# Kernel tuning notes

Hardware: AMD Instinct MI355X
Metric: run time of the kernel (lower is better)

Reference implementation:

```python
import jax, jax.numpy as jnp
import numpy as np
import math

B, T, D, H = 2, 2048, 1024, 16


def _layernorm(x, gamma, beta, eps=1e-5):
    mu = jnp.mean(x, axis=-1, keepdims=True)
    var = jnp.var(x, axis=-1, keepdims=True)
    return (x - mu) * jax.lax.rsqrt(var + eps) * gamma + beta


def setup_inputs() -> dict:
    key = jax.random.key(0)
    ks = jax.random.split(key, 12)
    s = 1.0 / math.sqrt(D)
    return {
        "x": jax.random.normal(ks[0], (B, T, D), dtype=jnp.float32),
        "src_mask": jax.random.randint(ks[1], (B, T, T), 0, 2, dtype=jnp.int32),
        "ln_gamma": jnp.ones((D,), jnp.float32),
        "ln_beta": jnp.zeros((D,), jnp.float32),
        "Wq": jax.random.normal(ks[2], (D, D), jnp.float32) * s,
        "bq": jnp.zeros((D,), jnp.float32),
        "Wk": jax.random.normal(ks[3], (D, D), jnp.float32) * s,
        "bk": jnp.zeros((D,), jnp.float32),
        "Wv": jax.random.normal(ks[4], (D, D), jnp.float32) * s,
        "bv": jnp.zeros((D,), jnp.float32),
        "Wo": jax.random.normal(ks[5], (D, D), jnp.float32) * s,
        "bo": jnp.zeros((D,), jnp.float32),
    }


def reference(x, src_mask, ln_gamma, ln_beta, Wq, bq, Wk, bk, Wv, bv, Wo, bo):
    Bx, Tx, Dx = x.shape
    dh = Dx // H
    xn = _layernorm(x, ln_gamma, ln_beta)  # single LN; the three calls are identical
    q = (xn @ Wq + bq).reshape(Bx, Tx, H, dh)
    k = (xn @ Wk + bk).reshape(Bx, Tx, H, dh)
    v = (xn @ Wv + bv).reshape(Bx, Tx, H, dh)
    # scores: B, n, m, h
    attn = jnp.einsum('bnhd,bmhd->bnmh', q, k) / math.sqrt(dh)
    attn = attn + (1.0 - src_mask.astype(attn.dtype))[..., None] * -100000.0
    weight = jax.nn.softmax(attn, axis=2)
    y = jnp.einsum('bnmh,bmhd->bnhd', weight, v).reshape(Bx, Tx, Dx)
    return x + (y @ Wo + bo)
```

## Files before the change

kernel.cpp:

```cpp
#include <hip/hip_runtime.h>
#include <hip/hip_bf16.h>
#include <stdint.h>

#define Tq 2048
#define Dd 1024
#define Hh 16

typedef unsigned short u16;
typedef __attribute__((ext_vector_type(8))) short short8;
typedef __attribute__((ext_vector_type(4))) float f32x4;

__device__ __forceinline__ u16 f2bf(float f) {
  union { float f; unsigned u; } v; v.f = f;
  unsigned r = (v.u + 0x7fffu + ((v.u >> 16) & 1u)) >> 16;
  return (u16)r;
}

__device__ __forceinline__ unsigned pk2bf(float a, float b) {
  __hip_bfloat162 h = __float22bfloat162_rn(float2{a, b});
  union { __hip_bfloat162 h; unsigned u; } c; c.h = h;
  return c.u;
}

__device__ __forceinline__ void load_lds16(const void* g, void* l) {
  __builtin_amdgcn_global_load_lds(
      (const __attribute__((address_space(1))) unsigned*)g,
      (__attribute__((address_space(3))) unsigned*)l, 16, 0, 0);
}

__device__ __forceinline__ f32x4 mfma16(short8 a, short8 b, f32x4 c) {
  return __builtin_amdgcn_mfma_f32_16x16x32_bf16(a, b, c, 0, 0, 0);
}

__device__ __forceinline__ void permswap(unsigned& xx, unsigned& yy) {
#if __has_builtin(__builtin_amdgcn_permlane32_swap) && \
    __has_builtin(__builtin_amdgcn_permlane16_swap)
  typedef __attribute__((ext_vector_type(2))) unsigned uint2v;
  uint2v t0 = __builtin_amdgcn_permlane32_swap(xx, yy, false, false);
  uint2v t1 = __builtin_amdgcn_permlane16_swap(t0[0], t0[1], false, false);
  xx = t1[0];
  yy = t1[1];
#else
  asm volatile(
      "s_nop 1\n\t"
      "v_permlane32_swap_b32 %0, %1\n\t"
      "s_nop 1\n\t"
      "v_permlane16_swap_b32 %0, %1\n\t"
      "s_nop 1"
      : "+v"(xx), "+v"(yy));
#endif
}

__global__ __launch_bounds__(256) void prep_kernel(
    const float* __restrict__ x, const float* __restrict__ gamma,
    const float* __restrict__ beta, u16* __restrict__ xn,
    const float* __restrict__ W0, const float* __restrict__ W1,
    const float* __restrict__ W2, const float* __restrict__ W3,
    u16* __restrict__ o_qkv, u16* __restrict__ o_o,
    const int* __restrict__ mask, uint32_t* __restrict__ bits,
    const float* __restrict__ bq, const float* __restrict__ bk,
    const float* __restrict__ bv, float* __restrict__ bias3) {
  __shared__ float t[32][33];
  int idx = blockIdx.x;
  int tid = threadIdx.x;
  if (idx < 4096) {
    int row = idx;
    const float4 v = ((const float4*)(x + (size_t)row * Dd))[tid];
    float s = v.x + v.y + v.z + v.w;
    float s2 = v.x * v.x + v.y * v.y + v.z * v.z + v.w * v.w;
#pragma unroll
    for (int off = 1; off < 64; off <<= 1) {
      s += __shfl_xor(s, off);
      s2 += __shfl_xor(s2, off);
    }
    int w = tid >> 6;
    if ((tid & 63) == 0) { t[0][w] = s; t[0][4 + w] = s2; }
    __syncthreads();
    s = t[0][0] + t[0][1] + t[0][2] + t[0][3];
    s2 = t[0][4] + t[0][5] + t[0][6] + t[0][7];
    float mu = s * (1.0f / Dd);
    float var = s2 * (1.0f / Dd) - mu * mu;
    float rstd = rsqrtf(var + 1e-5f);
    const float4 g = ((const float4*)gamma)[tid];
    const float4 bb = ((const float4*)beta)[tid];
    union { unsigned us[2]; uint2 u2; } o;
    o.us[0] = pk2bf((v.x - mu) * rstd * g.x + bb.x, (v.y - mu) * rstd * g.y + bb.y);
    o.us[1] = pk2bf((v.z - mu) * rstd * g.z + bb.z, (v.w - mu) * rstd * g.w + bb.w);
    *(uint2*)(xn + (size_t)row * Dd + tid * 4) = o.u2;
  } else if (idx < 8192) {
    int ti = idx - 4096;
    int z = ti >> 10, i = ti & 1023;
    const float* W = (z == 0) ? W0 : (z == 1) ? W1 : (z == 2) ? W2 : W3;
    u16* out = (z < 3) ? (o_qkv + (size_t)z * 1024 * 1024) : o_o;
    int k0 = (i & 31) * 32, n0 = (i >> 5) * 32;
    int tx = tid & 31, ty = tid >> 5;
#pragma unroll
    for (int j = 0; j < 4; ++j)
      t[ty + j * 8][tx] = W[(size_t)(k0 + ty + j * 8) * Dd + n0 + tx];
    __syncthreads();
#pragma unroll
    for (int j = 0; j < 4; ++j)
      out[(size_t)(n0 + ty + j * 8) * Dd + k0 + tx] = f2bf(t[tx][ty + j * 8]);
  } else if (idx < 9216) {
    int m = idx - 8192;
    int b = m >> 9, rest = m & 511;
    int qw = rest >> 3, kblk = rest & 7;
    int k = kblk * 256 + tid;
    const int* mp = mask + ((size_t)b * Tq + qw * 32) * Tq + k;
    uint32_t wv = 0;
#pragma unroll
    for (int j = 0; j < 32; ++j) wv |= (mp[(size_t)j * Tq] ? 1u : 0u) << j;
    bits[((size_t)b * 64 + qw) * Tq + k] = wv;
  } else {
    int i = (idx - 9216) * 256 + tid;
    float v = (i < 1024) ? bq[i] : (i < 2048) ? bk[i - 1024] : bv[i - 2048];
    bias3[i] = v;
  }
}

__global__ __launch_bounds__(256) void qkvt_gemm(
    const u16* __restrict__ xn, const u16* __restrict__ wt,
    const float* __restrict__ bias3, u16* __restrict__ qkvb,
    u16* __restrict__ vtb) {
  __shared__ u16 As[128 * 32];
  __shared__ u16 Bs[128 * 32];
  int bid = blockIdx.x;
  bool vmode = bid >= 512;
  int m0, n0, ldc;
  const u16 *A, *Bt;
  u16* C;
  if (!vmode) {
    m0 = (bid >> 4) * 128; n0 = (bid & 15) * 128;
    A = xn; Bt = wt; C = qkvb; ldc = 2048;
  } else {
    int ti = bid - 512;
    m0 = (ti >> 5) * 128; n0 = (ti & 31) * 128;
    A = wt + (size_t)2 * 1024 * 1024; Bt = xn; C = vtb; ldc = 4096;
  }
  int tid = threadIdx.x;
  int lane = tid & 63, w = tid >> 6;
  int l16 = lane & 15, quad = lane >> 4;
  int wm = w >> 1, wn = w & 1;
  int srow = lane >> 2, scol = (lane & 3) << 3;
  const u16* ga0 = A + (size_t)(m0 + srow) * 1024 + scol;
  const u16* gb0 = Bt + (size_t)(n0 + srow) * 1024 + scol;
  f32x4 acc[4][4];
#pragma unroll
  for (int i = 0; i < 4; ++i)
#pragma unroll
    for (int j = 0; j < 4; ++j) acc[i][j] = {0.f, 0.f, 0.f, 0.f};

  for (int k0 = 0; k0 < 1024; k0 += 32) {
    __syncthreads();
#pragma unroll
    for (int c = 0; c < 2; ++c) {
      int rb = w * 32 + c * 16;
      load_lds16(ga0 + (size_t)rb * 1024 + k0, (char*)As + rb * 64);
      load_lds16(gb0 + (size_t)rb * 1024 + k0, (char*)Bs + rb * 64);
    }
    __syncthreads();
    short8 af[4], bf[4];
#pragma unroll
    for (int mt = 0; mt < 4; ++mt)
      af[mt] = *(const short8*)&As[(wm * 64 + mt * 16 + l16) * 32 + quad * 8];
#pragma unroll
    for (int nt = 0; nt < 4; ++nt)
      bf[nt] = *(const short8*)&Bs[(wn * 64 + nt * 16 + l16) * 32 + quad * 8];
#pragma unroll
    for (int mt = 0; mt < 4; ++mt)
#pragma unroll
      for (int nt = 0; nt < 4; ++nt)
        acc[mt][nt] = mfma16(af[mt], bf[nt], acc[mt][nt]);
  }
#pragma unroll
  for (int nt = 0; nt < 4; ++nt) {
    int col = n0 + wn * 64 + nt * 16 + l16;
    float bcol = vmode ? 0.f : bias3[col];
    float scl = (!vmode && col < 1024) ? 0.18033688011112042f : 1.0f;
#pragma unroll
    for (int mt = 0; mt < 4; ++mt) {
#pragma unroll
      for (int r = 0; r < 4; ++r) {
        int row = m0 + wm * 64 + mt * 16 + quad * 4 + r;
        float bv = vmode ? bias3[2048 + row] : bcol;
        C[(size_t)row * ldc + col] = f2bf((acc[mt][nt][r] + bv) * scl);
      }
    }
  }
}

template <int MT>
__global__ __launch_bounds__(256) void gemm_bt(
    const u16* __restrict__ A, const u16* __restrict__ Bt,
    const float* __restrict__ bias, const float* __restrict__ resid,
    float* __restrict__ Cout, int ldc, int K) {
  constexpr int MTI = MT / 32;
  constexpr int ACALLS = MT / 64;
  __shared__ u16 As[MT * 32];
  __shared__ u16 Bs[128 * 32];
  int tid = threadIdx.x;
  int lane = tid & 63, w = tid >> 6;
  int l16 = lane & 15, quad = lane >> 4;
  int wm = w >> 1, wn = w & 1;
  int m0 = blockIdx.y * MT, n0 = blockIdx.x * 128;
  int srow = lane >> 2, scol = (lane & 3) << 3;
  const u16* ga0 = A + (size_t)(m0 + srow) * K + scol;
  const u16* gb0 = Bt + (size_t)(n0 + srow) * K + scol;
  f32x4 acc[MTI][4];
#pragma unroll
  for (int i = 0; i < MTI; ++i)
#pragma unroll
    for (int j = 0; j < 4; ++j) acc[i][j] = {0.f, 0.f, 0.f, 0.f};

  for (int k0 = 0; k0 < K; k0 += 32) {
    __syncthreads();
#pragma unroll
    for (int c = 0; c < ACALLS; ++c) {
      int rb = w * (MT / 4) + c * 16;
      load_lds16(ga0 + (size_t)rb * K + k0, (char*)As + rb * 64);
    }
#pragma unroll
    for (int c = 0; c < 2; ++c) {
      int rb = w * 32 + c * 16;
      load_lds16(gb0 + (size_t)rb * K + k0, (char*)Bs + rb * 64);
    }
    __syncthreads();
    short8 af[MTI], bf[4];
#pragma unroll
    for (int mt = 0; mt < MTI; ++mt)
      af[mt] = *(const short8*)&As[(wm * (MT / 2) + mt * 16 + l16) * 32 + quad * 8];
#pragma unroll
    for (int nt = 0; nt < 4; ++nt)
      bf[nt] = *(const short8*)&Bs[(wn * 64 + nt * 16 + l16) * 32 + quad * 8];
#pragma unroll
    for (int mt = 0; mt < MTI; ++mt)
#pragma unroll
      for (int nt = 0; nt < 4; ++nt)
        acc[mt][nt] = mfma16(af[mt], bf[nt], acc[mt][nt]);
  }
#pragma unroll
  for (int nt = 0; nt < 4; ++nt) {
    int col = n0 + wn * 64 + nt * 16 + l16;
    float bv = bias[col];
#pragma unroll
    for (int mt = 0; mt < MTI; ++mt) {
#pragma unroll
      for (int r = 0; r < 4; ++r) {
        int row = m0 + wm * (MT / 2) + mt * 16 + quad * 4 + r;
        size_t idx = (size_t)row * ldc + col;
        Cout[idx] = acc[mt][nt][r] + bv + resid[idx];
      }
    }
  }
}

__global__ __launch_bounds__(256, 4) void attn_kernel(
    const u16* __restrict__ qkv, const u16* __restrict__ vt,
    const uint32_t* __restrict__ mbits, u16* __restrict__ ybuf) {
  __shared__ u16 Ks[2][64 * 64];
  __shared__ u16 Vs[3][64 * 64];
  int tid = threadIdx.x;
  int lane = tid & 63, w = tid >> 6;
  int l16 = lane & 15, quad = lane >> 4;
  int x7 = l16 & 7;
  int qt = blockIdx.x, h = blockIdx.y, b = blockIdx.z;
  int qbase = qt * 64 + w * 16;
  const u16* Qb = qkv + (size_t)b * Tq * 2048 + h * 64;
  const u16* Kb = Qb + 1024;
  const u16* Vb = vt + (size_t)(h * 64) * 4096 + b * 2048;
  const uint32_t* Mrow = mbits + ((size_t)b * 64 + (qbase >> 5)) * Tq;
  int shift = (qbase & 31) + l16;

  int half = (w & 1) * 32;
  int r8 = lane >> 3;
  int phys = lane & 7;
  int chunk = phys ^ r8;
  bool isK = (w < 2);

  short8 qf[2];
#pragma unroll
  for (int ks = 0; ks < 2; ++ks)
    qf[ks] = *(const short8*)&Qb[(size_t)(qbase + l16) * 2048 + ks * 32 + quad * 8];

  const short8 vones = {0x3F80, 0x3F80, 0x3F80, 0x3F80,
                        0x3F80, 0x3F80, 0x3F80, 0x3F80};

  f32x4 acc[4];
#pragma unroll
  for (int j = 0; j < 4; ++j) acc[j] = {0.f, 0.f, 0.f, 0.f};
  f32x4 acc_s = {0.f, 0.f, 0.f, 0.f};

  auto stage = [&](int kb, int vb, int k0) {
    if (isK) {
#pragma unroll
      for (int j = 0; j < 4; ++j)
        load_lds16(Kb + (size_t)(k0 + half + j * 8 + r8) * 2048 + chunk * 8,
                   (char*)&Ks[kb][0] + (half + j * 8) * 128);
    } else {
#pragma unroll
      for (int j = 0; j < 4; ++j)
        load_lds16(Vb + (size_t)(half + j * 8 + r8) * 4096 + k0 + chunk * 8,
                   (char*)&Vs[vb][0] + (half + j * 8) * 128);
    }
  };

  auto ldmask = [&](int k0, uint32_t (&mv)[4][4]) {
#pragma unroll
    for (int mt = 0; mt < 4; ++mt) {
      uint4 m4 = *(const uint4*)&Mrow[k0 + mt * 16 + quad * 4];
      mv[mt][0] = m4.x; mv[mt][1] = m4.y; mv[mt][2] = m4.z; mv[mt][3] = m4.w;
    }
  };

  auto qk = [&](const u16* Kt, f32x4 (&s)[4]) {
#pragma unroll
    for (int i = 0; i < 4; ++i) s[i] = {0.f, 0.f, 0.f, 0.f};
#pragma unroll
    for (int mt = 0; mt < 4; ++mt)
#pragma unroll
      for (int ks = 0; ks < 2; ++ks) {
        short8 kf = *(const short8*)&Kt[(mt * 16 + l16) * 64 +
                                        (((ks << 2) | quad) ^ x7) * 8];
        s[mt] = mfma16(kf, qf[ks], s[mt]);
      }
  };

  auto softmax_pack = [&](f32x4 (&s)[4], uint32_t (&mv)[4][4],
                          short8 (&pfo)[2]) {
    unsigned c[4][2];
#pragma unroll
    for (int mt = 0; mt < 4; ++mt) {
      float p[4];
#pragma unroll
      for (int r = 0; r < 4; ++r) {
        float e = __builtin_amdgcn_exp2f(s[mt][r]);
        int keep = __builtin_amdgcn_sbfe((int)mv[mt][r], (unsigned)shift, 1u);
        union { float f; int i; } u; u.f = e; u.i &= keep;
        p[r] = u.f;
      }
      c[mt][0] = pk2bf(p[0], p[1]);
      c[mt][1] = pk2bf(p[2], p[3]);
    }
#pragma unroll
    for (int ks = 0; ks < 2; ++ks) {
      union { unsigned u[4]; short8 s8; } P;
#pragma unroll
      for (int hh = 0; hh < 2; ++hh) {
        unsigned xx = c[2 * ks][hh], yy = c[2 * ks + 1][hh];
        permswap(xx, yy);
        P.u[hh] = xx;
        P.u[2 + hh] = yy;
      }
      pfo[ks] = P.s8;
    }
  };

  auto pv = [&](const u16* Vtile, short8 (&pf)[2]) {
    acc_s = mfma16(pf[0], vones, acc_s);
    acc_s = mfma16(pf[1], vones, acc_s);
#pragma unroll
    for (int ks = 0; ks < 2; ++ks)
#pragma unroll
      for (int nt2 = 0; nt2 < 4; ++nt2) {
        short8 vf = *(const short8*)&Vtile[(nt2 * 16 + l16) * 64 +
                                           (((ks << 2) | quad) ^ x7) * 8];
        acc[nt2] = mfma16(pf[ks], vf, acc[nt2]);
      }
  };

  stage(0, 0, 0);
  __syncthreads();
  uint32_t mv[4][4];
  f32x4 s[4];
  short8 pfp[2];
  ldmask(0, mv);
  stage(1, 1, 64);
  __builtin_amdgcn_s_setprio(1);
  qk(Ks[0], s);
  __builtin_amdgcn_s_setprio(0);
  softmax_pack(s, mv, pfp);

  for (int kt = 1; kt < 32; ++kt) {
    int k0 = kt * 64;
    __syncthreads();
    ldmask(k0, mv);
    if (kt < 31) stage((kt + 1) & 1, (kt + 1) % 3, k0 + 64);
    __builtin_amdgcn_s_setprio(1);
    qk(Ks[kt & 1], s);
    pv(Vs[(kt - 1) % 3], pfp);
    __builtin_amdgcn_s_setprio(0);
    short8 pfc[2];
    softmax_pack(s, mv, pfc);
    pfp[0] = pfc[0];
    pfp[1] = pfc[1];
  }
  __builtin_amdgcn_s_setprio(1);
  pv(Vs[1], pfp);
  __builtin_amdgcn_s_setprio(0);

#pragma unroll
  for (int r = 0; r < 4; ++r) {
    float li = 1.0f / acc_s[r];
    size_t row = (size_t)b * Tq + qbase + quad * 4 + r;
#pragma unroll
    for (int nt2 = 0; nt2 < 4; ++nt2)
      ybuf[row * Dd + h * 64 + nt2 * 16 + l16] = f2bf(acc[nt2][r] * li);
  }
}

extern "C" void kernel_launch(void* const* d_in, const int* in_sizes, int n_in,
                              void* d_out, int out_size, void* d_ws, size_t ws_size,
                              hipStream_t stream) {
  (void)in_sizes; (void)n_in; (void)out_size; (void)ws_size;
  const float* x = (const float*)d_in[0];
  const int* mask = (const int*)d_in[1];
  const float* gamma = (const float*)d_in[2];
  const float* beta = (const float*)d_in[3];
  const float* Wq = (const float*)d_in[4];
  const float* bq = (const float*)d_in[5];
  const float* Wk = (const float*)d_in[6];
  const float* bk = (const float*)d_in[7];
  const float* Wv = (const float*)d_in[8];
  const float* bv = (const float*)d_in[9];
  const float* Wo = (const float*)d_in[10];
  const float* bo = (const float*)d_in[11];
  float* out = (float*)d_out;
  char* ws = (char*)d_ws;

  constexpr size_t SZ_XN = (size_t)4096 * 1024 * 2;
  constexpr size_t SZ_WTQ = (size_t)3072 * 1024 * 2;
  constexpr size_t SZ_WOT = (size_t)1024 * 1024 * 2;
  constexpr size_t SZ_B3 = 3072 * 4;
  constexpr size_t SZ_QKV = (size_t)4096 * 2048 * 2;
  constexpr size_t SZ_MBITS = (size_t)2 * 64 * 2048 * 4;
  constexpr size_t SZ_VT = (size_t)1024 * 4096 * 2;
  size_t off = 0;
  u16* xn = (u16*)(ws + off); off += SZ_XN;
  u16* wtqkv = (u16*)(ws + off); off += SZ_WTQ;
  u16* wot = (u16*)(ws + off); off += SZ_WOT;
  float* bias3 = (float*)(ws + off); off += SZ_B3;
  u16* qkvb = (u16*)(ws + off); off += SZ_QKV;
  uint32_t* mbits = (uint32_t*)(ws + off); off += SZ_MBITS;
  u16* vtb = (u16*)(ws + off); off += SZ_VT;
  u16* ybuf = (u16*)(ws + off);

  prep_kernel<<<dim3(9228), dim3(256), 0, stream>>>(
      x, gamma, beta, xn, Wq, Wk, Wv, Wo, wtqkv, wot, mask, mbits, bq, bk, bv,
      bias3);
  qkvt_gemm<<<dim3(768), dim3(256), 0, stream>>>(xn, wtqkv, bias3, qkvb, vtb);
  attn_kernel<<<dim3(32, 16, 2), dim3(256), 0, stream>>>(qkvb, vtb, mbits, ybuf);
  gemm_bt<64><<<dim3(8, 64), dim3(256), 0, stream>>>(
      ybuf, wot, bo, x, out, 1024, 1024);
}
```

Before: 240.0 us.

## Double-buffer LDS in GEMMs, remap QKV block order, vectorize mask packing

Both GEMM kernels now use two LDS buffers, so the next K-tile load is issued before computing on the current one, with a single barrier per iteration. The QKV GEMM also permutes block indices, likely to spread blocks across XCDs and improve L2 locality. The mask bit-packing now reads int4 per thread and writes uint4, which cuts the prep grid from 1024 mask blocks to 256. The cost is doubled LDS use per block, which may reduce occupancy, and fewer threads doing the mask pass.

Result: slower. 253.0 us (+5.4%).

```diff
diff --git a/kernel.cpp b/kernel.cpp
--- a/kernel.cpp
+++ b/kernel.cpp
@@ -101,18 +101,25 @@
 #pragma unroll
     for (int j = 0; j < 4; ++j)
       out[(size_t)(n0 + ty + j * 8) * Dd + k0 + tx] = f2bf(t[tx][ty + j * 8]);
-  } else if (idx < 9216) {
+  } else if (idx < 8448) {
     int m = idx - 8192;
-    int b = m >> 9, rest = m & 511;
-    int qw = rest >> 3, kblk = rest & 7;
-    int k = kblk * 256 + tid;
-    const int* mp = mask + ((size_t)b * Tq + qw * 32) * Tq + k;
-    uint32_t wv = 0;
-#pragma unroll
-    for (int j = 0; j < 32; ++j) wv |= (mp[(size_t)j * Tq] ? 1u : 0u) << j;
-    bits[((size_t)b * 64 + qw) * Tq + k] = wv;
+    int b = m >> 7, rest = m & 127;
+    int qw = rest >> 1, kblk = rest & 1;
+    int k4 = kblk * 1024 + tid * 4;
+    const int* mp = mask + ((size_t)b * Tq + qw * 32) * Tq + k4;
+    uint32_t wv0 = 0, wv1 = 0, wv2 = 0, wv3 = 0;
+#pragma unroll
+    for (int j = 0; j < 32; ++j) {
+      int4 m4 = *(const int4*)(mp + (size_t)j * Tq);
+      wv0 |= (m4.x ? 1u : 0u) << j;
+      wv1 |= (m4.y ? 1u : 0u) << j;
+      wv2 |= (m4.z ? 1u : 0u) << j;
+      wv3 |= (m4.w ? 1u : 0u) << j;
+    }
+    uint4 o4 = {wv0, wv1, wv2, wv3};
+    *(uint4*)&bits[((size_t)b * 64 + qw) * Tq + k4] = o4;
   } else {
-    int i = (idx - 9216) * 256 + tid;
+    int i = (idx - 8448) * 256 + tid;
     float v = (i < 1024) ? bq[i] : (i < 2048) ? bk[i - 1024] : bv[i - 2048];
     bias3[i] = v;
   }
@@ -122,9 +129,10 @@
     const u16* __restrict__ xn, const u16* __restrict__ wt,
     const float* __restrict__ bias3, u16* __restrict__ qkvb,
     u16* __restrict__ vtb) {
-  __shared__ u16 As[128 * 32];
-  __shared__ u16 Bs[128 * 32];
-  int bid = blockIdx.x;
+  __shared__ u16 As[2][128 * 32];
+  __shared__ u16 Bs[2][128 * 32];
+  int b0 = blockIdx.x;
+  int bid = (b0 & 7) * 96 + (b0 >> 3);
   bool vmode = bid >= 512;
   int m0, n0, ldc;
   const u16 *A, *Bt;
@@ -150,27 +158,33 @@
 #pragma unroll
     for (int j = 0; j < 4; ++j) acc[i][j] = {0.f, 0.f, 0.f, 0.f};
 
-  for (int k0 = 0; k0 < 1024; k0 += 32) {
-    __syncthreads();
+  auto stage = [&](int buf, int k0) {
 #pragma unroll
     for (int c = 0; c < 2; ++c) {
       int rb = w * 32 + c * 16;
-      load_lds16(ga0 + (size_t)rb * 1024 + k0, (char*)As + rb * 64);
-      load_lds16(gb0 + (size_t)rb * 1024 + k0, (char*)Bs + rb * 64);
-    }
-    __syncthreads();
+      load_lds16(ga0 + (size_t)rb * 1024 + k0, (char*)&As[buf][0] + rb * 64);
+      load_lds16(gb0 + (size_t)rb * 1024 + k0, (char*)&Bs[buf][0] + rb * 64);
+    }
+  };
+
+  stage(0, 0);
+  __syncthreads();
+  for (int kt = 0; kt < 32; ++kt) {
+    int buf = kt & 1;
+    if (kt < 31) stage(buf ^ 1, kt * 32 + 32);
     short8 af[4], bf[4];
 #pragma unroll
     for (int mt = 0; mt < 4; ++mt)
-      af[mt] = *(const short8*)&As[(wm * 64 + mt * 16 + l16) * 32 + quad * 8];
+      af[mt] = *(const short8*)&As[buf][(wm * 64 + mt * 16 + l16) * 32 + quad * 8];
 #pragma unroll
     for (int nt = 0; nt < 4; ++nt)
-      bf[nt] = *(const short8*)&Bs[(wn * 64 + nt * 16 + l16) * 32 + quad * 8];
+      bf[nt] = *(const short8*)&Bs[buf][(wn * 64 + nt * 16 + l16) * 32 + quad * 8];
 #pragma unroll
     for (int mt = 0; mt < 4; ++mt)
 #pragma unroll
       for (int nt = 0; nt < 4; ++nt)
         acc[mt][nt] = mfma16(af[mt], bf[nt], acc[mt][nt]);
+    __syncthreads();
   }
 #pragma unroll
   for (int nt = 0; nt < 4; ++nt) {
@@ -196,8 +210,8 @@
     float* __restrict__ Cout, int ldc, int K) {
   constexpr int MTI = MT / 32;
   constexpr int ACALLS = MT / 64;
-  __shared__ u16 As[MT * 32];
-  __shared__ u16 Bs[128 * 32];
+  __shared__ u16 As[2][MT * 32];
+  __shared__ u16 Bs[2][128 * 32];
   int tid = threadIdx.x;
   int lane = tid & 63, w = tid >> 6;
   int l16 = lane & 15, quad = lane >> 4;
@@ -212,31 +226,39 @@
 #pragma unroll
     for (int j = 0; j < 4; ++j) acc[i][j] = {0.f, 0.f, 0.f, 0.f};
 
-  for (int k0 = 0; k0 < K; k0 += 32) {
-    __syncthreads();
+  auto stage = [&](int buf, int k0) {
 #pragma unroll
     for (int c = 0; c < ACALLS; ++c) {
       int rb = w * (MT / 4) + c * 16;
-      load_lds16(ga0 + (size_t)rb * K + k0, (char*)As + rb * 64);
+      load_lds16(ga0 + (size_t)rb * K + k0, (char*)&As[buf][0] + rb * 64);
     }
 #pragma unroll
     for (int c = 0; c < 2; ++c) {
       int rb = w * 32 + c * 16;
-      load_lds16(gb0 + (size_t)rb * K + k0, (char*)Bs + rb * 64);
-    }
-    __syncthreads();
+      load_lds16(gb0 + (size_t)rb * K + k0, (char*)&Bs[buf][0] + rb * 64);
+    }
+  };
+
+  stage(0, 0);
+  __syncthreads();
+  int buf = 0;
+  for (int k0 = 0; k0 < K; k0 += 32) {
+    if (k0 + 32 < K) stage(buf ^ 1, k0 + 32);
     short8 af[MTI], bf[4];
 #pragma unroll
     for (int mt = 0; mt < MTI; ++mt)
-      af[mt] = *(const short8*)&As[(wm * (MT / 2) + mt * 16 + l16) * 32 + quad * 8];
+      af[mt] =
+          *(const short8*)&As[buf][(wm * (MT / 2) + mt * 16 + l16) * 32 + quad * 8];
 #pragma unroll
     for (int nt = 0; nt < 4; ++nt)
-      bf[nt] = *(const short8*)&Bs[(wn * 64 + nt * 16 + l16) * 32 + quad * 8];
+      bf[nt] = *(const short8*)&Bs[buf][(wn * 64 + nt * 16 + l16) * 32 + quad * 8];
 #pragma unroll
     for (int mt = 0; mt < MTI; ++mt)
 #pragma unroll
       for (int nt = 0; nt < 4; ++nt)
         acc[mt][nt] = mfma16(af[mt], bf[nt], acc[mt][nt]);
+    __syncthreads();
+    buf ^= 1;
   }
 #pragma unroll
   for (int nt = 0; nt < 4; ++nt) {
@@ -444,7 +466,7 @@
   u16* vtb = (u16*)(ws + off); off += SZ_VT;
   u16* ybuf = (u16*)(ws + off);
 
-  prep_kernel<<<dim3(9228), dim3(256), 0, stream>>>(
+  prep_kernel<<<dim3(8460), dim3(256), 0, stream>>>(
       x, gamma, beta, xn, Wq, Wk, Wv, Wo, wtqkv, wot, mask, mbits, bq, bk, bv,
       bias3);
   qkvt_gemm<<<dim3(768), dim3(256), 0, stream>>>(xn, wtqkv, bias3, qkvb, vtb);
```

## Switch attention kernel to 32x32x16 MFMA with two-wave blocks of 32 query rows

Applied to the files above, without the earlier changes.

Rewrites the attention kernel to use 32x32x16 bf16 MFMA tiles. Each wave now owns 32 query rows, and the block shrinks from four waves to two, with one wave staging K and the other V. The goal is fewer MFMA issues and fewer LDS fragment reads per unit of work, plus a single permlane32 swap instead of two permlane swaps. The cost is larger accumulator register footprint, fewer waves per block and less occupancy, with each staging wave now issuing twice as many loads.

Result: slower. 246.4 us (+2.7%).

```diff
diff --git a/kernel.cpp b/kernel.cpp
--- a/kernel.cpp
+++ b/kernel.cpp
@@ -9,6 +9,7 @@
 typedef unsigned short u16;
 typedef __attribute__((ext_vector_type(8))) short short8;
 typedef __attribute__((ext_vector_type(4))) float f32x4;
+typedef __attribute__((ext_vector_type(16))) float f32x16;
 
 __device__ __forceinline__ u16 f2bf(float f) {
   union { float f; unsigned u; } v; v.f = f;
@@ -32,22 +33,22 @@
   return __builtin_amdgcn_mfma_f32_16x16x32_bf16(a, b, c, 0, 0, 0);
 }
 
-__device__ __forceinline__ void permswap(unsigned& xx, unsigned& yy) {
-#if __has_builtin(__builtin_amdgcn_permlane32_swap) && \
-    __has_builtin(__builtin_amdgcn_permlane16_swap)
+__device__ __forceinline__ f32x16 mfma32(short8 a, short8 b, f32x16 c) {
+  return __builtin_amdgcn_mfma_f32_32x32x16_bf16(a, b, c, 0, 0, 0);
+}
+
+__device__ __forceinline__ void swap32(unsigned& a, unsigned& b) {
+#if __has_builtin(__builtin_amdgcn_permlane32_swap)
   typedef __attribute__((ext_vector_type(2))) unsigned uint2v;
-  uint2v t0 = __builtin_amdgcn_permlane32_swap(xx, yy, false, false);
-  uint2v t1 = __builtin_amdgcn_permlane16_swap(t0[0], t0[1], false, false);
-  xx = t1[0];
-  yy = t1[1];
+  uint2v t = __builtin_amdgcn_permlane32_swap(a, b, false, false);
+  a = t[0];
+  b = t[1];
 #else
   asm volatile(
       "s_nop 1\n\t"
       "v_permlane32_swap_b32 %0, %1\n\t"
-      "s_nop 1\n\t"
-      "v_permlane16_swap_b32 %0, %1\n\t"
       "s_nop 1"
-      : "+v"(xx), "+v"(yy));
+      : "+v"(a), "+v"(b));
 #endif
 }
 
@@ -254,125 +255,134 @@
   }
 }
 
-__global__ __launch_bounds__(256, 4) void attn_kernel(
+__global__ __launch_bounds__(128, 2) void attn_kernel(
     const u16* __restrict__ qkv, const u16* __restrict__ vt,
     const uint32_t* __restrict__ mbits, u16* __restrict__ ybuf) {
   __shared__ u16 Ks[2][64 * 64];
   __shared__ u16 Vs[3][64 * 64];
   int tid = threadIdx.x;
   int lane = tid & 63, w = tid >> 6;
-  int l16 = lane & 15, quad = lane >> 4;
-  int x7 = l16 & 7;
+  int l31 = lane & 31, hi = lane >> 5;
+  int x7 = l31 & 7;
   int qt = blockIdx.x, h = blockIdx.y, b = blockIdx.z;
-  int qbase = qt * 64 + w * 16;
+  int qbase = qt * 64 + w * 32;
   const u16* Qb = qkv + (size_t)b * Tq * 2048 + h * 64;
   const u16* Kb = Qb + 1024;
   const u16* Vb = vt + (size_t)(h * 64) * 4096 + b * 2048;
   const uint32_t* Mrow = mbits + ((size_t)b * 64 + (qbase >> 5)) * Tq;
-  int shift = (qbase & 31) + l16;
-
-  int half = (w & 1) * 32;
+
   int r8 = lane >> 3;
   int phys = lane & 7;
   int chunk = phys ^ r8;
-  bool isK = (w < 2);
-
-  short8 qf[2];
-#pragma unroll
-  for (int ks = 0; ks < 2; ++ks)
-    qf[ks] = *(const short8*)&Qb[(size_t)(qbase + l16) * 2048 + ks * 32 + quad * 8];
+  bool isK = (w == 0);
+
+  short8 qf[4];
+#pragma unroll
+  for (int ks = 0; ks < 4; ++ks)
+    qf[ks] =
+        *(const short8*)&Qb[(size_t)(qbase + l31) * 2048 + ks * 16 + hi * 8];
 
   const short8 vones = {0x3F80, 0x3F80, 0x3F80, 0x3F80,
                         0x3F80, 0x3F80, 0x3F80, 0x3F80};
 
-  f32x4 acc[4];
-#pragma unroll
-  for (int j = 0; j < 4; ++j) acc[j] = {0.f, 0.f, 0.f, 0.f};
-  f32x4 acc_s = {0.f, 0.f, 0.f, 0.f};
+  f32x16 acc[2], acc_s;
+#pragma unroll
+  for (int i = 0; i < 16; ++i) {
+    acc[0][i] = 0.f;
+    acc[1][i] = 0.f;
+    acc_s[i] = 0.f;
+  }
 
   auto stage = [&](int kb, int vb, int k0) {
     if (isK) {
 #pragma unroll
-      for (int j = 0; j < 4; ++j)
-        load_lds16(Kb + (size_t)(k0 + half + j * 8 + r8) * 2048 + chunk * 8,
-                   (char*)&Ks[kb][0] + (half + j * 8) * 128);
+      for (int j = 0; j < 8; ++j)
+        load_lds16(Kb + (size_t)(k0 + j * 8 + r8) * 2048 + chunk * 8,
+                   (char*)&Ks[kb][0] + j * 1024);
     } else {
 #pragma unroll
-      for (int j = 0; j < 4; ++j)
-        load_lds16(Vb + (size_t)(half + j * 8 + r8) * 4096 + k0 + chunk * 8,
-                   (char*)&Vs[vb][0] + (half + j * 8) * 128);
+      for (int j = 0; j < 8; ++j)
+        load_lds16(Vb + (size_t)(j * 8 + r8) * 4096 + k0 + chunk * 8,
+                   (char*)&Vs[vb][0] + j * 1024);
     }
   };
 
-  auto ldmask = [&](int k0, uint32_t (&mv)[4][4]) {
-#pragma unroll
-    for (int mt = 0; mt < 4; ++mt) {
-      uint4 m4 = *(const uint4*)&Mrow[k0 + mt * 16 + quad * 4];
-      mv[mt][0] = m4.x; mv[mt][1] = m4.y; mv[mt][2] = m4.z; mv[mt][3] = m4.w;
-    }
+  auto ldmask = [&](int k0, uint4 (&mv)[2][4]) {
+#pragma unroll
+    for (int t = 0; t < 2; ++t)
+#pragma unroll
+      for (int g = 0; g < 4; ++g)
+        mv[t][g] = *(const uint4*)&Mrow[k0 + t * 32 + g * 8 + hi * 4];
   };
 
-  auto qk = [&](const u16* Kt, f32x4 (&s)[4]) {
-#pragma unroll
-    for (int i = 0; i < 4; ++i) s[i] = {0.f, 0.f, 0.f, 0.f};
-#pragma unroll
-    for (int mt = 0; mt < 4; ++mt)
-#pragma unroll
-      for (int ks = 0; ks < 2; ++ks) {
-        short8 kf = *(const short8*)&Kt[(mt * 16 + l16) * 64 +
-                                        (((ks << 2) | quad) ^ x7) * 8];
-        s[mt] = mfma16(kf, qf[ks], s[mt]);
-      }
+  auto qk = [&](const u16* Kt, f32x16 (&s)[2]) {
+#pragma unroll
+    for (int t = 0; t < 2; ++t) {
+#pragma unroll
+      for (int i = 0; i < 16; ++i) s[t][i] = 0.f;
+#pragma unroll
+      for (int ks = 0; ks < 4; ++ks) {
+        short8 kf = *(const short8*)&Kt[(t * 32 + l31) * 64 +
+                                        ((ks * 2 + hi) ^ x7) * 8];
+        s[t] = mfma32(kf, qf[ks], s[t]);
+      }
+    }
   };
 
-  auto softmax_pack = [&](f32x4 (&s)[4], uint32_t (&mv)[4][4],
-                          short8 (&pfo)[2]) {
-    unsigned c[4][2];
-#pragma unroll
-    for (int mt = 0; mt < 4; ++mt) {
-      float p[4];
-#pragma unroll
-      for (int r = 0; r < 4; ++r) {
-        float e = __builtin_amdgcn_exp2f(s[mt][r]);
-        int keep = __builtin_amdgcn_sbfe((int)mv[mt][r], (unsigned)shift, 1u);
-        union { float f; int i; } u; u.f = e; u.i &= keep;
-        p[r] = u.f;
-      }
-      c[mt][0] = pk2bf(p[0], p[1]);
-      c[mt][1] = pk2bf(p[2], p[3]);
-    }
-#pragma unroll
-    for (int ks = 0; ks < 2; ++ks) {
-      union { unsigned u[4]; short8 s8; } P;
-#pragma unroll
-      for (int hh = 0; hh < 2; ++hh) {
-        unsigned xx = c[2 * ks][hh], yy = c[2 * ks + 1][hh];
-        permswap(xx, yy);
-        P.u[hh] = xx;
-        P.u[2 + hh] = yy;
-      }
-      pfo[ks] = P.s8;
+  auto softmax_pack = [&](f32x16 (&s)[2], uint4 (&mv)[2][4], short8 (&pf)[4]) {
+#pragma unroll
+    for (int t = 0; t < 2; ++t) {
+      float p[16];
+#pragma unroll
+      for (int g = 0; g < 4; ++g) {
+        uint32_t mw0 = mv[t][g].x, mw1 = mv[t][g].y;
+        uint32_t mw2 = mv[t][g].z, mw3 = mv[t][g].w;
+        uint32_t mws[4] = {mw0, mw1, mw2, mw3};
+#pragma unroll
+        for (int i = 0; i < 4; ++i) {
+          int r = g * 4 + i;
+          float e = __builtin_amdgcn_exp2f(s[t][r]);
+          int keep = __builtin_amdgcn_sbfe((int)mws[i], (unsigned)l31, 1u);
+          union { float f; int i_; } u;
+          u.f = e;
+          u.i_ &= keep;
+          p[r] = u.f;
+        }
+      }
+#pragma unroll
+      for (int sl = 0; sl < 2; ++sl) {
+        int g0 = 2 * sl;
+        unsigned w0 = pk2bf(p[4 * g0 + 0], p[4 * g0 + 1]);
+        unsigned w1 = pk2bf(p[4 * g0 + 2], p[4 * g0 + 3]);
+        unsigned w2 = pk2bf(p[4 * g0 + 4], p[4 * g0 + 5]);
+        unsigned w3 = pk2bf(p[4 * g0 + 6], p[4 * g0 + 7]);
+        swap32(w0, w2);
+        swap32(w1, w3);
+        union { unsigned u[4]; short8 s8; } P;
+        P.u[0] = w0; P.u[1] = w1; P.u[2] = w2; P.u[3] = w3;
+        pf[2 * t + sl] = P.s8;
+      }
     }
   };
 
-  auto pv = [&](const u16* Vtile, short8 (&pf)[2]) {
-    acc_s = mfma16(pf[0], vones, acc_s);
-    acc_s = mfma16(pf[1], vones, acc_s);
-#pragma unroll
-    for (int ks = 0; ks < 2; ++ks)
-#pragma unroll
-      for (int nt2 = 0; nt2 < 4; ++nt2) {
-        short8 vf = *(const short8*)&Vtile[(nt2 * 16 + l16) * 64 +
-                                           (((ks << 2) | quad) ^ x7) * 8];
-        acc[nt2] = mfma16(pf[ks], vf, acc[nt2]);
-      }
+  auto pv = [&](const u16* Vtile, short8 (&pf)[4]) {
+#pragma unroll
+    for (int ss = 0; ss < 4; ++ss) {
+      acc_s = mfma32(pf[ss], vones, acc_s);
+#pragma unroll
+      for (int dt = 0; dt < 2; ++dt) {
+        short8 vf = *(const short8*)&Vtile[(dt * 32 + l31) * 64 +
+                                           ((ss * 2 + hi) ^ x7) * 8];
+        acc[dt] = mfma32(pf[ss], vf, acc[dt]);
+      }
+    }
   };
 
   stage(0, 0, 0);
   __syncthreads();
-  uint32_t mv[4][4];
-  f32x4 s[4];
-  short8 pfp[2];
+  uint4 mv[2][4];
+  f32x16 s[2];
+  short8 pfp[4];
   ldmask(0, mv);
   stage(1, 1, 64);
   __builtin_amdgcn_s_setprio(1);
@@ -389,22 +399,23 @@
     qk(Ks[kt & 1], s);
     pv(Vs[(kt - 1) % 3], pfp);
     __builtin_amdgcn_s_setprio(0);
-    short8 pfc[2];
+    short8 pfc[4];
     softmax_pack(s, mv, pfc);
-    pfp[0] = pfc[0];
-    pfp[1] = pfc[1];
+#pragma unroll
+    for (int i = 0; i < 4; ++i) pfp[i] = pfc[i];
   }
   __builtin_amdgcn_s_setprio(1);
   pv(Vs[1], pfp);
   __builtin_amdgcn_s_setprio(0);
 
 #pragma unroll
-  for (int r = 0; r < 4; ++r) {
+  for (int r = 0; r < 16; ++r) {
     float li = 1.0f / acc_s[r];
-    size_t row = (size_t)b * Tq + qbase + quad * 4 + r;
-#pragma unroll
-    for (int nt2 = 0; nt2 < 4; ++nt2)
-      ybuf[row * Dd + h * 64 + nt2 * 16 + l16] = f2bf(acc[nt2][r] * li);
+    int qr = (r & 3) + 8 * (r >> 2) + 4 * hi;
+    size_t row = (size_t)b * Tq + qbase + qr;
+#pragma unroll
+    for (int dt = 0; dt < 2; ++dt)
+      ybuf[row * Dd + h * 64 + dt * 32 + l31] = f2bf(acc[dt][r] * li);
   }
 }
 
@@ -448,7 +459,7 @@
       x, gamma, beta, xn, Wq, Wk, Wv, Wo, wtqkv, wot, mask, mbits, bq, bk, bv,
       bias3);
   qkvt_gemm<<<dim3(768), dim3(256), 0, stream>>>(xn, wtqkv, bias3, qkvb, vtb);
-  attn_kernel<<<dim3(32, 16, 2), dim3(256), 0, stream>>>(qkvb, vtb, mbits, ybuf);
+  attn_kernel<<<dim3(32, 16, 2), dim3(128), 0, stream>>>(qkvb, vtb, mbits, ybuf);
   gemm_bt<64><<<dim3(8, 64), dim3(256), 0, stream>>>(
       ybuf, wot, bo, x, out, 1024, 1024);
 }
```
